# Optimization experiments

Hardware: AMD Instinct MI355X
Metric: run time of the kernel (lower is better)

Reference implementation:

```python
import jax, jax.numpy as jnp
import numpy as np

N_NODES = 50000


def setup_inputs() -> dict:
    key = jax.random.key(0)
    ks = jax.random.split(key, 9)
    x = jax.random.normal(ks[0], (N_NODES, 32), dtype=jnp.float32)
    pos = jax.random.normal(ks[1], (N_NODES, 3), dtype=jnp.float32)
    edge_index = jax.random.randint(ks[2], (2, 1600000), 0, N_NODES, dtype=jnp.int64)
    W1 = jax.random.normal(ks[3], (35, 64), dtype=jnp.float32) * 0.1
    b1 = jnp.zeros((64,), dtype=jnp.float32)
    W2 = jax.random.normal(ks[4], (64, 64), dtype=jnp.float32) * 0.1
    b2 = jnp.zeros((64,), dtype=jnp.float32)
    Wg = jax.random.normal(ks[5], (64, 128), dtype=jnp.float32) * 0.1
    bg = jnp.zeros((128,), dtype=jnp.float32)
    return {"x": x, "pos": pos, "edge_index": edge_index,
            "W1": W1, "b1": b1, "W2": W2, "b2": b2, "Wg": Wg, "bg": bg}


def reference(x, pos, edge_index, W1, b1, W2, b2, Wg, bg):
    N = x.shape[0]
    # add_self_loops=True: append (i, i) edges
    self_idx = jnp.arange(N, dtype=edge_index.dtype)
    src = jnp.concatenate([edge_index[0], self_idx])  # message source j
    dst = jnp.concatenate([edge_index[1], self_idx])  # aggregation target i
    # message: concat(x_j, pos_j - pos_i) -> local_nn (Lin+ReLU x2)
    msg = jnp.concatenate([x[src], pos[src] - pos[dst]], axis=-1)  # [E+N, 35]
    h = jax.nn.relu(msg @ W1 + b1)  # [E+N, 64]
    h = jax.nn.relu(h @ W2 + b2)    # [E+N, 64]
    # max aggregation per destination node (self loops guarantee nonempty segments)
    agg = jax.ops.segment_max(h, dst, num_segments=N)  # [N, 64]
    # global_nn: Linear
    return agg @ Wg + bg  # [N, 128]
```

## Files before the change

kernel.cpp:

```cpp
#include <hip/hip_runtime.h>

#define N_NODES 50000
#define N_EDGES 1600000
#define N_TOTAL (N_EDGES + N_NODES)
#define F_IN    32
#define HID     64
#define F_OUT   128
#define G       32
#define NB      1563
#define CAP1_MAX 1408
#define OVF_CAP 16384
#define W1WIN   4096
#define NBINBLK  403
#define NNODEBLK 196
#define NPAIR   782

#define OFF_QBF   0
#define OFF_CUR1  (N_NODES * 32)
#define OFF_OVFC  (OFF_CUR1 + NB * 16)
#define OFF_OVF   (OFF_OVFC + 16)
#define OFF_BIN   (OFF_OVF + OVF_CAP)
#define NCLR      (NB * 16 + 16)

typedef __attribute__((ext_vector_type(2))) _Float16 h2f;
typedef __attribute__((ext_vector_type(8))) _Float16 half8;
typedef __attribute__((ext_vector_type(4))) float v4f;

__device__ __forceinline__ unsigned f2h2(float a, float b) {
    h2f v;
    v.x = (_Float16)a; v.y = (_Float16)b;
    return __builtin_bit_cast(unsigned, v);
}

__device__ __forceinline__ unsigned hsubmax0(unsigned a, unsigned b) {
    h2f x = __builtin_bit_cast(h2f, a) - __builtin_bit_cast(h2f, b);
    h2f z = {(_Float16)0.f, (_Float16)0.f};
    x = __builtin_elementwise_max(x, z);
    return __builtin_bit_cast(unsigned, x);
}

__device__ __forceinline__ float h2lo(unsigned u) { return (float)__builtin_bit_cast(h2f, u).x; }
__device__ __forceinline__ float h2hi(unsigned u) { return (float)__builtin_bit_cast(h2f, u).y; }
__device__ __forceinline__ float f16r(float x)    { return (float)(_Float16)x; }

#define WAVE_FENCE() do { asm volatile("s_waitcnt lgkmcnt(0)" ::: "memory"); \
                          __builtin_amdgcn_sched_barrier(0); } while (0)

__global__ __launch_bounds__(256) void zero_kernel(unsigned* __restrict__ clr)
{
    const int i = blockIdx.x * 256 + threadIdx.x;
    if (i < NCLR) clr[i] = 0u;
}

__global__ __launch_bounds__(1024) void bin_pre_kernel(
    const int* __restrict__ ei,
    unsigned* __restrict__ cur1, unsigned* __restrict__ bin1,
    unsigned* __restrict__ ovfc, unsigned* __restrict__ ovf, int cap1,
    const float* __restrict__ x, const float* __restrict__ pos,
    const float* __restrict__ W1, const float* __restrict__ b1,
    unsigned* __restrict__ qbf)
{
    __shared__ unsigned stage[W1WIN];
    __shared__ unsigned hist[NB + 1];
    __shared__ unsigned startp[NB + 1];
    __shared__ unsigned gbase[NB];
    __shared__ unsigned wpart[16];
    __shared__ float    w1s[35 * HID + HID];

    const int t = threadIdx.x, lane = t & 63;

    if (blockIdx.x >= NBINBLK) {
        for (int i = t; i < 35 * HID; i += 1024) w1s[i] = W1[i];
        if (t < HID) w1s[35 * HID + t] = b1[t];
        __syncthreads();

        const int n = (blockIdx.x - NBINBLK) * 256 + (t >> 2);
        const int sub = t & 3;
        if (n >= N_NODES) return;

        const float4* x4 = (const float4*)(x + (long long)n * F_IN);
        const float4 xa = x4[sub * 2], xb = x4[sub * 2 + 1];
        const float xv[8] = {xa.x, xa.y, xa.z, xa.w, xb.x, xb.y, xb.z, xb.w};

        float acc[16];
        #pragma unroll
        for (int k = 0; k < 16; ++k) acc[k] = w1s[35 * HID + sub * 16 + k];

        #pragma unroll
        for (int c = 0; c < F_IN; ++c) {
            const float xm = __shfl(xv[c & 7], (lane & 60) | (c >> 3), 64);
            #pragma unroll
            for (int k = 0; k < 16; ++k)
                acc[k] = fmaf(xm, w1s[c * HID + sub * 16 + k], acc[k]);
        }
        #pragma unroll
        for (int a = 0; a < 3; ++a) {
            const float pp = pos[n * 3 + a];
            #pragma unroll
            for (int k = 0; k < 16; ++k)
                acc[k] = fmaf(pp, w1s[(F_IN + a) * HID + sub * 16 + k], acc[k]);
        }

        uint4* o4 = (uint4*)(qbf + (unsigned)n * 32u + (unsigned)sub * 8u);
        o4[0] = make_uint4(f2h2(acc[0], acc[1]),  f2h2(acc[2], acc[3]),
                           f2h2(acc[4], acc[5]),  f2h2(acc[6], acc[7]));
        o4[1] = make_uint4(f2h2(acc[8], acc[9]),  f2h2(acc[10], acc[11]),
                           f2h2(acc[12], acc[13]), f2h2(acc[14], acc[15]));
        return;
    }

    const int wbase = blockIdx.x * W1WIN;

    for (int i = t; i < NB + 1; i += 1024) hist[i] = 0u;
    __syncthreads();

    unsigned ev[4]; int bv[4]; unsigned rv[4]; bool val[4];
    #pragma unroll
    for (int k = 0; k < 4; ++k) {
        const int idx = wbase + k * 1024 + t;
        val[k] = idx < N_TOTAL;
        if (val[k]) {
            int s, d;
            if (idx < N_EDGES) { s = ei[idx]; d = ei[N_EDGES + idx]; }
            else               { s = d = idx - N_EDGES; }
            ev[k] = ((unsigned)d << 16) | (unsigned)s;
            bv[k] = d >> 5;
            rv[k] = atomicAdd(&hist[bv[k]], 1u);
        }
    }
    __syncthreads();

    unsigned h0 = 0, hpair = 0;
    if (t < NPAIR) { h0 = hist[2 * t]; hpair = h0 + hist[2 * t + 1]; }
    unsigned v = hpair;
    #pragma unroll
    for (int o = 1; o < 64; o <<= 1) {
        const unsigned u = __shfl_up(v, o, 64);
        if (lane >= o) v += u;
    }
    if (lane == 63) wpart[t >> 6] = v;
    __syncthreads();
    if (t == 0) {
        unsigned r = 0;
        #pragma unroll
        for (int i = 0; i < 16; ++i) { const unsigned c2 = wpart[i]; wpart[i] = r; r += c2; }
        startp[NB] = r;
    }
    __syncthreads();
    if (t < NPAIR) {
        const unsigned bse = (v - hpair) + wpart[t >> 6];
        startp[2 * t]     = bse;
        startp[2 * t + 1] = bse + h0;
    }
    for (int i = t; i < NB; i += 1024)
        if (hist[i]) gbase[i] = atomicAdd(&cur1[i * 16], hist[i]);
    __syncthreads();

    #pragma unroll
    for (int k = 0; k < 4; ++k)
        if (val[k]) stage[startp[bv[k]] + rv[k]] = ev[k];
    __syncthreads();

    const unsigned total = startp[NB];
    for (unsigned i = t; i < total; i += 1024u) {
        const unsigned e = stage[i];
        const unsigned b = e >> 21;
        const unsigned gp = gbase[b] + (i - startp[b]);
        if (gp < (unsigned)cap1) bin1[b * (unsigned)cap1 + gp] = e;
        else {
            const unsigned qo = atomicAdd(ovfc, 1u);
            if (qo < OVF_CAP) ovf[qo] = e;
        }
    }
}

__global__ __launch_bounds__(256, 4) void gather_kernel(
    const unsigned* __restrict__ qbf,
    const float* __restrict__ pos,
    const unsigned* __restrict__ cur1,
    const unsigned* __restrict__ bkt,
    int cap1,
    const float* __restrict__ W1p,
    const float* __restrict__ W2, const float* __restrict__ b2,
    float* __restrict__ out)
{
    __shared__ unsigned aggs[(G + 1) * HID];
    __shared__ unsigned rlds[G * 32];
    __shared__ unsigned ast[4][64 * 16];

    const int t = threadIdx.x, lane = t & 63, w = t >> 6;
    const int q = lane >> 4, m15 = lane & 15;
    const int b = blockIdx.x;
    const unsigned cnt  = min(cur1[b * 16], (unsigned)cap1);
    const unsigned base = (unsigned)b * (unsigned)cap1;

    for (int i = t; i < (G + 1) * HID; i += 256) aggs[i] = 0u;
    for (int i = t; i < G * 32; i += 256) {
        const int dl = i >> 5, k2 = i & 31;
        const int node = b * G + dl;
        float v0 = 0.f, v1 = 0.f;
        if (node < N_NODES) {
            #pragma unroll
            for (int a = 0; a < 3; ++a) {
                const float pp = pos[node * 3 + a];
                v0 = fmaf(pp, W1p[a * HID + 2 * k2], v0);
                v1 = fmaf(pp, W1p[a * HID + 2 * k2 + 1], v1);
            }
        }
        rlds[(dl << 5) + ((((k2 >> 2) ^ (dl & 7)) << 2) | (k2 & 3))] = f2h2(v0, v1);
    }

    half8 bfr[2][2][2];
    #pragma unroll
    for (int h = 0; h < 2; ++h)
        #pragma unroll
        for (int ntl = 0; ntl < 2; ++ntl) {
            const int nn = (2 * h + ntl) * 16 + m15;
            #pragma unroll
            for (int ks = 0; ks < 2; ++ks) {
                half8 vv;
                #pragma unroll
                for (int j = 0; j < 4; ++j) {
                    const int ku = (ks * 4 + q) * 4 + j;
                    vv[2 * j]     = (_Float16)W2[(2 * ku) * HID + nn];
                    vv[2 * j + 1] = (_Float16)W2[(2 * ku + 1) * HID + nn];
                }
                bfr[h][ntl][ks] = vv;
            }
        }
    float b2v[4];
    #pragma unroll
    for (int nt = 0; nt < 4; ++nt) b2v[nt] = b2[nt * 16 + m15];
    __syncthreads();

    unsigned* aw = ast[w];
    const int axw = ((lane >> 1) & 3) << 2;
    const int axr = ((m15 >> 1) & 3) << 2;
    const unsigned nit = (cnt + 255u) >> 8;

    #pragma unroll 1
    for (unsigned it = 0; it < nit; ++it) {
        const unsigned off = it * 256u + (unsigned)w * 64u;
        const unsigned rem = (off < cnt) ? min(64u, cnt - off) : 0u;
        const unsigned f = off + (unsigned)lane;
        unsigned pent = 0u;
        if (f < cnt) pent = bkt[base + f];
        const int s = (int)(pent & 0xFFFFu), dl = (int)((pent >> 16) & 31u);

        const uint4* qr = (const uint4*)(qbf + (unsigned)s * 32u);
        const int rbase = dl << 5, rx = dl & 7;

        half8 a0[4], a1[4];

        uint4 qva[4];
        #pragma unroll
        for (int i = 0; i < 4; ++i) qva[i] = qr[i];

        uint4 hh0[4];
        #pragma unroll
        for (int j4 = 0; j4 < 4; ++j4) {
            const uint4 r4 = *(const uint4*)(rlds + rbase + ((j4 ^ rx) << 2));
            hh0[j4].x = hsubmax0(qva[j4].x, r4.x);
            hh0[j4].y = hsubmax0(qva[j4].y, r4.y);
            hh0[j4].z = hsubmax0(qva[j4].z, r4.z);
            hh0[j4].w = hsubmax0(qva[j4].w, r4.w);
        }
        uint4 qvb[4];
        #pragma unroll
        for (int i = 0; i < 4; ++i) qvb[i] = qr[i + 4];

        #pragma unroll
        for (int j4 = 0; j4 < 4; ++j4)
            *(uint4*)(aw + (lane << 4) + ((j4 << 2) ^ axw)) = hh0[j4];
        WAVE_FENCE();
        #pragma unroll
        for (int mt = 0; mt < 4; ++mt)
            a0[mt] = *(const half8*)(
                aw + ((mt * 16 + m15) << 4) + ((q << 2) ^ axr));
        WAVE_FENCE();

        #pragma unroll
        for (int j4 = 0; j4 < 4; ++j4) {
            const uint4 r4 = *(const uint4*)(
                rlds + rbase + (((4 + j4) ^ rx) << 2));
            uint4 hh;
            hh.x = hsubmax0(qvb[j4].x, r4.x);
            hh.y = hsubmax0(qvb[j4].y, r4.y);
            hh.z = hsubmax0(qvb[j4].z, r4.z);
            hh.w = hsubmax0(qvb[j4].w, r4.w);
            *(uint4*)(aw + (lane << 4) + ((j4 << 2) ^ axw)) = hh;
        }
        WAVE_FENCE();
        #pragma unroll
        for (int mt = 0; mt < 4; ++mt)
            a1[mt] = *(const half8*)(
                aw + ((mt * 16 + m15) << 4) + ((q << 2) ^ axr));
        WAVE_FENCE();

        #pragma unroll
        for (int h = 0; h < 2; ++h) {
            v4f c[4][2];
            #pragma unroll
            for (int mt = 0; mt < 4; ++mt)
                #pragma unroll
                for (int ntl = 0; ntl < 2; ++ntl) {
                    const float bb2 = b2v[2 * h + ntl];
                    c[mt][ntl] = (v4f){bb2, bb2, bb2, bb2};
                }
            #pragma unroll
            for (int mt = 0; mt < 4; ++mt)
                #pragma unroll
                for (int ntl = 0; ntl < 2; ++ntl) {
                    c[mt][ntl] = __builtin_amdgcn_mfma_f32_16x16x32_f16(
                        a0[mt], bfr[h][ntl][0], c[mt][ntl], 0, 0, 0);
                    c[mt][ntl] = __builtin_amdgcn_mfma_f32_16x16x32_f16(
                        a1[mt], bfr[h][ntl][1], c[mt][ntl], 0, 0, 0);
                }
            #pragma unroll
            for (int mt = 0; mt < 4; ++mt)
                #pragma unroll
                for (int r = 0; r < 4; ++r) {
                    const int er = mt * 16 + q * 4 + r;
                    const int dv = __shfl(dl, er, 64);
                    const int dle = ((unsigned)er < rem) ? dv : G;
                    const int ab = (dle << 6) + m15;
                    #pragma unroll
                    for (int ntl = 0; ntl < 2; ++ntl) {
                        const float hv = fmaxf(c[mt][ntl][r], 0.f);
                        atomicMax(&aggs[ab + (2 * h + ntl) * 16],
                                  __float_as_uint(hv));
                    }
                }
        }
    }

    __syncthreads();
    for (int i = t; i < G * HID; i += 256) {
        const int row = i >> 6, ch = i & 63, n = b * G + row;
        if (n < N_NODES)
            out[(long long)n * F_OUT + HID + ch] = __uint_as_float(aggs[i]);
    }
}

__global__ __launch_bounds__(64) void ovf_kernel(
    const unsigned* __restrict__ qbf, const float* __restrict__ pos,
    const unsigned* __restrict__ ovfc, const unsigned* __restrict__ ovf,
    const float* __restrict__ W1p, const float* __restrict__ W2,
    const float* __restrict__ b2, unsigned* __restrict__ aggbits)
{
    const unsigned n = min(*ovfc, (unsigned)OVF_CAP);
    for (unsigned i = blockIdx.x * 64 + threadIdx.x; i < n; i += gridDim.x * 64) {
        const unsigned p = ovf[i];
        const int s = (int)(p & 0xFFFFu), d = (int)(p >> 16);
        float h1[HID];
        #pragma unroll 1
        for (int k = 0; k < HID; ++k) {
            const unsigned u = qbf[s * 32 + (k >> 1)];
            const float qp = (k & 1) ? h2hi(u) : h2lo(u);
            float r = 0.f;
            #pragma unroll 1
            for (int a = 0; a < 3; ++a) r = fmaf(pos[d * 3 + a], W1p[a * HID + k], r);
            h1[k] = fmaxf(f16r(qp - f16r(r)), 0.f);
        }
        unsigned* ap = aggbits + (long long)d * F_OUT + HID;
        #pragma unroll 1
        for (int k = 0; k < HID; ++k) {
            float a2 = b2[k];
            #pragma unroll 1
            for (int j = 0; j < HID; ++j)
                a2 = fmaf(h1[j], f16r(W2[j * HID + k]), a2);
            a2 = fmaxf(a2, 0.f);
            atomicMax(ap + k, __float_as_uint(a2));
        }
    }
}

__global__ __launch_bounds__(256) void out_gemm_kernel(
    float* __restrict__ out,
    const float* __restrict__ Wg,
    const float* __restrict__ bg)
{
    const int lane = threadIdx.x & 63;
    const int wave = blockIdx.x * (blockDim.x >> 6) + (threadIdx.x >> 6);
    const int nwav = gridDim.x * (blockDim.x >> 6);

    float w1r[HID], w2r[HID];
    #pragma unroll
    for (int j = 0; j < HID; ++j) {
        w1r[j] = Wg[j * F_OUT + lane];
        w2r[j] = Wg[j * F_OUT + 64 + lane];
    }
    const float bga = bg[lane];
    const float bgb = bg[64 + lane];

    for (int n = wave; n < N_NODES; n += nwav) {
        float* row = out + (long long)n * F_OUT;
        const float a = row[64 + lane];
        float y1 = bga, y2 = bgb;
        #pragma unroll
        for (int j = 0; j < HID; ++j) {
            const float aj = __shfl(a, j, 64);
            y1 = fmaf(aj, w1r[j], y1);
            y2 = fmaf(aj, w2r[j], y2);
        }
        row[lane]      = y1;
        row[64 + lane] = y2;
    }
}

extern "C" void kernel_launch(void* const* d_in, const int* in_sizes, int n_in,
                              void* d_out, int out_size, void* d_ws, size_t ws_size,
                              hipStream_t stream) {
    const float* x   = (const float*)d_in[0];
    const float* pos = (const float*)d_in[1];
    const int*   ei  = (const int*)d_in[2];
    const float* W1  = (const float*)d_in[3];
    const float* b1  = (const float*)d_in[4];
    const float* W2  = (const float*)d_in[5];
    const float* b2  = (const float*)d_in[6];
    const float* Wg  = (const float*)d_in[7];
    const float* bg  = (const float*)d_in[8];
    float* out = (float*)d_out;

    unsigned* ws    = (unsigned*)d_ws;
    unsigned* qbf   = ws + OFF_QBF;
    unsigned* cur1  = ws + OFF_CUR1;
    unsigned* ovfc  = ws + OFF_OVFC;
    unsigned* ovf   = ws + OFF_OVF;
    unsigned* bin1  = ws + OFF_BIN;

    long long avail = (long long)(ws_size / 4) - OFF_BIN;
    int cap1 = (int)(avail / NB);
    if (cap1 > CAP1_MAX) cap1 = CAP1_MAX;
    if (cap1 < 1152) cap1 = 1152;

    zero_kernel<<<(NCLR + 255) / 256, 256, 0, stream>>>(cur1);
    bin_pre_kernel<<<NBINBLK + NNODEBLK, 1024, 0, stream>>>(
        ei, cur1, bin1, ovfc, ovf, cap1, x, pos, W1, b1, qbf);
    gather_kernel<<<NB, 256, 0, stream>>>(
        qbf, pos, cur1, bin1, cap1, W1 + F_IN * HID, W2, b2, out);
    ovf_kernel<<<32, 64, 0, stream>>>(
        qbf, pos, ovfc, ovf, W1 + F_IN * HID, W2, b2, (unsigned*)out);
    out_gemm_kernel<<<512, 256, 0, stream>>>(out, Wg, bg);
}
```

Baseline: 220.0 us.

## Coarsen edge bins to 128 nodes and sub-filter per gather block into LDS queue

Edge binning now uses 392 coarse bins of 128 destination nodes instead of 1563 bins of 32, which shrinks the histogram and scan in the binning kernel and lowers global atomic contention. Each gather block scans its whole coarse bin, keeps the edges that belong to its 32-node sub-bin through a ballot-compacted shared-memory queue, and sends queue overflow to the existing overflow path. The aim is cheaper binning and better-filled bins. The cost is that every gather block reads its coarse bin four times over and uses extra LDS, which may lower occupancy.

```diff
diff --git a/kernel.cpp b/kernel.cpp
--- a/kernel.cpp
+++ b/kernel.cpp
@@ -8,19 +8,20 @@
 #define F_OUT   128
 #define G       32
 #define NB      1563
-#define CAP1_MAX 1408
+#define NBIN    392
+#define CAP1_MAX 5120
+#define QCAP    1536
 #define OVF_CAP 16384
 #define W1WIN   4096
 #define NBINBLK  403
 #define NNODEBLK 196
-#define NPAIR   782
 
 #define OFF_QBF   0
 #define OFF_CUR1  (N_NODES * 32)
-#define OFF_OVFC  (OFF_CUR1 + NB * 16)
+#define OFF_OVFC  (OFF_CUR1 + NBIN * 16)
 #define OFF_OVF   (OFF_OVFC + 16)
 #define OFF_BIN   (OFF_OVF + OVF_CAP)
-#define NCLR      (NB * 16 + 16)
+#define NCLR      (NBIN * 16 + 16)
 
 typedef __attribute__((ext_vector_type(2))) _Float16 h2f;
 typedef __attribute__((ext_vector_type(8))) _Float16 half8;
@@ -61,9 +62,7 @@
     unsigned* __restrict__ qbf)
 {
     __shared__ unsigned stage[W1WIN];
-    __shared__ unsigned hist[NB + 1];
-    __shared__ unsigned startp[NB + 1];
-    __shared__ unsigned gbase[NB];
+    __shared__ unsigned hist[NBIN], startp[NBIN + 1], gbase[NBIN];
     __shared__ unsigned wpart[16];
     __shared__ float    w1s[35 * HID + HID];
 
@@ -111,7 +110,7 @@
 
     const int wbase = blockIdx.x * W1WIN;
 
-    for (int i = t; i < NB + 1; i += 1024) hist[i] = 0u;
+    for (int i = t; i < NBIN; i += 1024) hist[i] = 0u;
     __syncthreads();
 
     unsigned ev[4]; int bv[4]; unsigned rv[4]; bool val[4];
@@ -124,36 +123,31 @@
             if (idx < N_EDGES) { s = ei[idx]; d = ei[N_EDGES + idx]; }
             else               { s = d = idx - N_EDGES; }
             ev[k] = ((unsigned)d << 16) | (unsigned)s;
-            bv[k] = d >> 5;
+            bv[k] = d >> 7;
             rv[k] = atomicAdd(&hist[bv[k]], 1u);
         }
     }
     __syncthreads();
 
-    unsigned h0 = 0, hpair = 0;
-    if (t < NPAIR) { h0 = hist[2 * t]; hpair = h0 + hist[2 * t + 1]; }
-    unsigned v = hpair;
+    unsigned hv = 0;
+    if (t < NBIN) hv = hist[t];
+    unsigned v = hv;
     #pragma unroll
     for (int o = 1; o < 64; o <<= 1) {
         const unsigned u = __shfl_up(v, o, 64);
-        if (lane >= o) v += u;
-    }
-    if (lane == 63) wpart[t >> 6] = v;
+        if ((t & 63) >= o) v += u;
+    }
+    if ((t & 63) == 63) wpart[t >> 6] = v;
     __syncthreads();
     if (t == 0) {
         unsigned r = 0;
         #pragma unroll
         for (int i = 0; i < 16; ++i) { const unsigned c2 = wpart[i]; wpart[i] = r; r += c2; }
-        startp[NB] = r;
-    }
-    __syncthreads();
-    if (t < NPAIR) {
-        const unsigned bse = (v - hpair) + wpart[t >> 6];
-        startp[2 * t]     = bse;
-        startp[2 * t + 1] = bse + h0;
-    }
-    for (int i = t; i < NB; i += 1024)
-        if (hist[i]) gbase[i] = atomicAdd(&cur1[i * 16], hist[i]);
+        startp[NBIN] = r;
+    }
+    __syncthreads();
+    if (t < NBIN) startp[t] = (v - hv) + wpart[t >> 6];
+    if (t < NBIN && hv) gbase[t] = atomicAdd(&cur1[t * 16], hv);
     __syncthreads();
 
     #pragma unroll
@@ -161,10 +155,10 @@
         if (val[k]) stage[startp[bv[k]] + rv[k]] = ev[k];
     __syncthreads();
 
-    const unsigned total = startp[NB];
+    const unsigned total = startp[NBIN];
     for (unsigned i = t; i < total; i += 1024u) {
         const unsigned e = stage[i];
-        const unsigned b = e >> 21;
+        const unsigned b = e >> 23;
         const unsigned gp = gbase[b] + (i - startp[b]);
         if (gp < (unsigned)cap1) bin1[b * (unsigned)cap1 + gp] = e;
         else {
@@ -180,6 +174,7 @@
     const unsigned* __restrict__ cur1,
     const unsigned* __restrict__ bkt,
     int cap1,
+    unsigned* __restrict__ ovfc, unsigned* __restrict__ ovf,
     const float* __restrict__ W1p,
     const float* __restrict__ W2, const float* __restrict__ b2,
     float* __restrict__ out)
@@ -187,13 +182,17 @@
     __shared__ unsigned aggs[(G + 1) * HID];
     __shared__ unsigned rlds[G * 32];
     __shared__ unsigned ast[4][64 * 16];
+    __shared__ unsigned queue[QCAP];
+    __shared__ unsigned qcnt;
 
     const int t = threadIdx.x, lane = t & 63, w = t >> 6;
     const int q = lane >> 4, m15 = lane & 15;
     const int b = blockIdx.x;
-    const unsigned cnt  = min(cur1[b * 16], (unsigned)cap1);
-    const unsigned base = (unsigned)b * (unsigned)cap1;
-
+    const int bin = b >> 2, sb = b & 3;
+    const unsigned cntb = min(cur1[bin * 16], (unsigned)cap1);
+    const unsigned gb = (unsigned)bin * (unsigned)cap1;
+
+    if (t == 0) qcnt = 0u;
     for (int i = t; i < (G + 1) * HID; i += 256) aggs[i] = 0u;
     for (int i = t; i < G * 32; i += 256) {
         const int dl = i >> 5, k2 = i & 31;
@@ -208,6 +207,34 @@
             }
         }
         rlds[(dl << 5) + ((((k2 >> 2) ^ (dl & 7)) << 2) | (k2 & 3))] = f2h2(v0, v1);
+    }
+    __syncthreads();
+
+    {
+        const unsigned nit2 = (cntb + 255u) >> 8;
+        for (unsigned it = 0; it < nit2; ++it) {
+            const unsigned idx = it * 256u + (unsigned)t;
+            unsigned e = 0u; bool mine = false;
+            if (idx < cntb) {
+                e = bkt[gb + idx];
+                mine = (((e >> 21) & 3u) == (unsigned)sb);
+            }
+            const unsigned long long bal = __ballot(mine);
+            const unsigned rank =
+                (unsigned)__popcll(bal & ((1ull << lane) - 1ull));
+            unsigned wb = 0u;
+            if (lane == 0 && bal)
+                wb = atomicAdd(&qcnt, (unsigned)__popcll(bal));
+            wb = __shfl(wb, 0, 64);
+            if (mine) {
+                const unsigned p = wb + rank;
+                if (p < QCAP) queue[p] = e;
+                else {
+                    const unsigned qo = atomicAdd(ovfc, 1u);
+                    if (qo < OVF_CAP) ovf[qo] = e;
+                }
+            }
+        }
     }
 
     half8 bfr[2][2][2];
@@ -233,6 +260,8 @@
     for (int nt = 0; nt < 4; ++nt) b2v[nt] = b2[nt * 16 + m15];
     __syncthreads();
 
+    const unsigned cnt = min(qcnt, (unsigned)QCAP);
+
     unsigned* aw = ast[w];
     const int axw = ((lane >> 1) & 3) << 2;
     const int axr = ((m15 >> 1) & 3) << 2;
@@ -244,7 +273,7 @@
         const unsigned rem = (off < cnt) ? min(64u, cnt - off) : 0u;
         const unsigned f = off + (unsigned)lane;
         unsigned pent = 0u;
-        if (f < cnt) pent = bkt[base + f];
+        if (f < cnt) pent = queue[f];
         const int s = (int)(pent & 0xFFFFu), dl = (int)((pent >> 16) & 31u);
 
         const uint4* qr = (const uint4*)(qbf + (unsigned)s * 32u);
@@ -430,15 +459,16 @@
     unsigned* bin1  = ws + OFF_BIN;
 
     long long avail = (long long)(ws_size / 4) - OFF_BIN;
-    int cap1 = (int)(avail / NB);
+    int cap1 = (int)(avail / NBIN);
     if (cap1 > CAP1_MAX) cap1 = CAP1_MAX;
-    if (cap1 < 1152) cap1 = 1152;
+    if (cap1 < 2048) cap1 = 2048;
 
     zero_kernel<<<(NCLR + 255) / 256, 256, 0, stream>>>(cur1);
     bin_pre_kernel<<<NBINBLK + NNODEBLK, 1024, 0, stream>>>(
         ei, cur1, bin1, ovfc, ovf, cap1, x, pos, W1, b1, qbf);
     gather_kernel<<<NB, 256, 0, stream>>>(
-        qbf, pos, cur1, bin1, cap1, W1 + F_IN * HID, W2, b2, out);
+        qbf, pos, cur1, bin1, cap1, ovfc, ovf,
+        W1 + F_IN * HID, W2, b2, out);
     ovf_kernel<<<32, 64, 0, stream>>>(
         qbf, pos, ovfc, ovf, W1 + F_IN * HID, W2, b2, (unsigned*)out);
     out_gemm_kernel<<<512, 256, 0, stream>>>(out, Wg, bg);
```

Measured after the change: 223.5 us. About the same (+1.6%).
